# Kernel optimization log

Hardware: AMD Instinct MI355X
Metric: run time of the kernel (lower is better)

Reference implementation:

```python
import jax, jax.numpy as jnp
import numpy as np

B, C_IN, C_OUT, N, K = 4, 128, 128, 4096, 32
BN_EPS = 1e-5


def setup_inputs() -> dict:
    key = jax.random.key(0)
    ks = jax.random.split(key, 12)
    x = jax.random.normal(ks[0], (B, C_IN, N), jnp.float32)
    feature = jax.random.normal(ks[1], (B, C_OUT, N, K), jnp.float32)
    graph_index = jax.random.randint(ks[2], (B, N, K), 0, N)
    s_in = 1.0 / np.sqrt(C_IN)
    s_out = 1.0 / np.sqrt(C_OUT)
    # theta_x: Conv2d(C_IN -> C_IN, 1x1), shared for theta and phi branches
    Wt = jax.random.uniform(ks[3], (C_IN, C_IN), jnp.float32, -s_in, s_in)
    bt = jax.random.uniform(ks[4], (C_IN,), jnp.float32, -s_in, s_in)
    # g: Conv2d(C_OUT -> C_OUT, 1x1)
    Wg = jax.random.uniform(ks[5], (C_OUT, C_OUT), jnp.float32, -s_out, s_out)
    bg = jax.random.uniform(ks[6], (C_OUT,), jnp.float32, -s_out, s_out)
    # W: Conv1d(C_OUT -> C_OUT, 1) followed by BatchNorm1d(C_OUT)
    Ww = jax.random.uniform(ks[7], (C_OUT, C_OUT), jnp.float32, -s_out, s_out)
    bw = jax.random.uniform(ks[8], (C_OUT,), jnp.float32, -s_out, s_out)
    gamma = jnp.ones((C_OUT,), jnp.float32)
    beta = jnp.zeros((C_OUT,), jnp.float32)
    return {"graph_index": graph_index, "x": x, "feature": feature,
            "Wt": Wt, "bt": bt, "Wg": Wg, "bg": bg,
            "Ww": Ww, "bw": bw, "gamma": gamma, "beta": beta}


def reference(graph_index, x, feature, Wt, bt, Wg, bg, Ww, bw, gamma, beta):
    b, c, n = x.shape
    # torch does x.contiguous().view(B, N, C) -> a reshape, not a transpose
    xr = x.reshape(b, n, c)                                   # [B,N,C]
    # index_points: per-batch gather of k neighbors
    batch_idx = jnp.arange(b)[:, None, None]
    nb = xr[batch_idx, graph_index]                           # [B,N,K,C]
    # theta_x 1x1 conv applied to centre and to neighbors (shared weights)
    theta = jnp.einsum('bnc,dc->bnd', xr, Wt) + bt            # [B,N,C]
    phi = jnp.einsum('bnkc,dc->bnkd', nb, Wt) + bt            # [B,N,K,C]
    # local attention logits over k neighbors, softmax over k
    logits = jnp.einsum('bnd,bnkd->bnk', theta, phi)          # [B,N,K]
    coef = jax.nn.softmax(logits, axis=-1)                    # [B,N,K]
    # g 1x1 conv on neighbor value features
    gx = jnp.einsum('bcnk,dc->bnkd', feature, Wg) + bg        # [B,N,K,Cout]
    # weighted aggregation over neighbors
    out = jnp.einsum('bnk,bnkd->bnd', coef, gx)               # [B,N,Cout]
    # W: 1x1 Conv1d then BatchNorm1d (training-mode batch stats)
    y = jnp.einsum('bnd,ed->ben', out, Ww) + bw[None, :, None]  # [B,Cout,N]
    mean = jnp.mean(y, axis=(0, 2), keepdims=True)
    var = jnp.var(y, axis=(0, 2), keepdims=True)
    z = (y - mean) * jax.lax.rsqrt(var + BN_EPS)
    z = z * gamma[None, :, None] + beta[None, :, None]
    return z
```

## Files before the change

kernel.cpp:

```cpp
#include <hip/hip_runtime.h>
#include <hip/hip_bf16.h>

#define BB 4
#define CC 128
#define NN 4096
#define KK 32
#define THETA_OFF 0
#define THETA_SZ  (BB*NN*CC)
#define AGG_OFF   (THETA_OFF + THETA_SZ)
#define AGG_SZ    (BB*NN*CC)
#define M_OFF     (AGG_OFF + AGG_SZ)
#define M_SZ      (CC*CC)
#define B2_OFF    (M_OFF + M_SZ)
#define COEF_OFF  (B2_OFF + 128)
#define COEF_SZ   (BB*NN*KK)
#define PART_OFF  (COEF_OFF + COEF_SZ)
#define PART_SZ   (512*256)
#define PART2_OFF (PART_OFF + PART_SZ)
#define PART2_SZ  (64*256)

__device__ __forceinline__ float dot4(float4 a, float4 b) {
    return a.x*b.x + a.y*b.y + a.z*b.z + a.w*b.w;
}

__device__ __forceinline__ void async_copy16(const float* g, float* l) {
    __builtin_amdgcn_global_load_lds(
        (const __attribute__((address_space(1))) void*)g,
        (__attribute__((address_space(3))) void*)l, 16, 0, 0);
}

__global__ __launch_bounds__(256) void kWT(const float* __restrict__ x,
                                           const float* __restrict__ Wt,
                                           const float* __restrict__ bt,
                                           const float* __restrict__ Ww,
                                           const float* __restrict__ Wg,
                                           const float* __restrict__ bg,
                                           const float* __restrict__ bw,
                                           float* __restrict__ theta,
                                           float* __restrict__ M,
                                           float* __restrict__ b2) {
    __shared__ float xr[32][132];
    __shared__ float wt[128][36];
    int t = threadIdx.x;
    if (blockIdx.x >= 512) {
        int bid2 = blockIdx.x - 512;
        if (bid2 < 64) {
            int e = bid2 * 2 + (t >> 7);
            int c = t & 127;
            float acc = 0.f;
#pragma unroll 8
            for (int d = 0; d < 128; ++d)
                acc += Ww[e*128 + d] * Wg[d*128 + c];
            M[e*128 + c] = acc;
        } else if (t < 128) {
            float acc = bw[t];
            for (int d = 0; d < 128; ++d)
                acc += Ww[t*128 + d] * bg[d];
            b2[t] = acc;
        }
        return;
    }
    long base = (long)blockIdx.x * (32 * 128);
#pragma unroll
    for (int r = 0; r < 4; ++r) {
        int f = (t + 256*r) * 4;
        int dn = f >> 7, c = f & 127;
        *(float4*)&xr[dn][c] = *(const float4*)(x + base + f);
    }
    float acc[4][4] = {};
    int e0 = t & 31, dn0 = (t >> 5) * 4;
    for (int cb = 0; cb < 4; ++cb) {
        __syncthreads();
#pragma unroll
        for (int r = 0; r < 4; ++r) {
            int f = (t + 256*r) * 4;
            int d = f >> 5, cc = f & 31;
            *(float4*)&wt[d][cc] = *(const float4*)(Wt + d*128 + cb*32 + cc);
        }
        __syncthreads();
#pragma unroll
        for (int q = 0; q < 8; ++q) {
            float4 a4[4], m4[4];
#pragma unroll
            for (int j = 0; j < 4; ++j) a4[j] = *(const float4*)&xr[dn0+j][cb*32 + q*4];
#pragma unroll
            for (int i = 0; i < 4; ++i) m4[i] = *(const float4*)&wt[e0 + 32*i][q*4];
#pragma unroll
            for (int i = 0; i < 4; ++i)
#pragma unroll
                for (int j = 0; j < 4; ++j)
                    acc[i][j] += dot4(a4[j], m4[i]);
        }
    }
    __syncthreads();
#pragma unroll
    for (int i = 0; i < 4; ++i) {
        float b = bt[e0 + 32*i];
#pragma unroll
        for (int j = 0; j < 4; ++j)
            xr[dn0 + j][e0 + 32*i] = acc[i][j] + b;
    }
    __syncthreads();
#pragma unroll
    for (int r = 0; r < 4; ++r) {
        int f = (t + 256*r) * 4;
        int dn = f >> 7, c = f & 127;
        *(float4*)(theta + base + f) = *(const float4*)&xr[dn][c];
    }
}

__global__ __launch_bounds__(256) void kA(const int* __restrict__ gi,
                                          const float* __restrict__ theta,
                                          float* __restrict__ coefG) {
    __shared__ float tc[8][132];
    __shared__ float logits[8][33];
    int t = threadIdx.x;
    int bid = (blockIdx.x & 7) * 256 + (blockIdx.x >> 3);
    long trow0 = (long)bid * 8;
    int b = bid >> 9;
    int k = t >> 3, l8 = t & 7;
    {
        int f = t * 4;
        int dn = f >> 7, c = f & 127;
        *(float4*)&tc[dn][c] = *(const float4*)(theta + trow0*128 + f);
    }
    int idxs[8];
#pragma unroll
    for (int dn = 0; dn < 8; ++dn)
        idxs[dn] = gi[(trow0 + dn) * KK + k];
    __syncthreads();
    const float* tbat = theta + (long)b * NN * CC;
#pragma unroll 2
    for (int dn = 0; dn < 8; ++dn) {
        const float* row = tbat + (long)idxs[dn] * CC;
        float p = 0.f;
#pragma unroll
        for (int j = 0; j < 4; ++j) {
            int c = j*32 + l8*4;
            float4 g = *(const float4*)(row + c);
            float4 tcv = *(const float4*)&tc[dn][c];
            p += dot4(g, tcv);
        }
        p += __shfl_xor(p, 1);
        p += __shfl_xor(p, 2);
        p += __shfl_xor(p, 4);
        if (l8 == 0) logits[dn][k] = p;
    }
    __syncthreads();
    if (t < 64) {
        int row = t >> 3;
        float l[4];
#pragma unroll
        for (int j = 0; j < 4; ++j) l[j] = logits[row][l8 + 8*j];
        float m = fmaxf(fmaxf(l[0], l[1]), fmaxf(l[2], l[3]));
        m = fmaxf(m, __shfl_xor(m, 1));
        m = fmaxf(m, __shfl_xor(m, 2));
        m = fmaxf(m, __shfl_xor(m, 4));
        float e[4]; float s = 0.f;
#pragma unroll
        for (int j = 0; j < 4; ++j) { e[j] = __expf(l[j] - m); s += e[j]; }
        s += __shfl_xor(s, 1);
        s += __shfl_xor(s, 2);
        s += __shfl_xor(s, 4);
        float inv = 1.0f / s;
#pragma unroll
        for (int j = 0; j < 4; ++j)
            coefG[(trow0 + row) * KK + l8 + 8*j] = e[j] * inv;
    }
}

__global__ __launch_bounds__(256) void kB(const float* __restrict__ coefG,
                                          const float* __restrict__ feat,
                                          float* __restrict__ aggG) {
    __shared__ float stage[4][2][32][32];
    __shared__ float aggL[32][36];
    int t = threadIdx.x;
    int cc4 = blockIdx.x & 3;
    int tile = blockIdx.x >> 2;
    int b = tile >> 7;
    int n0 = (tile & 127) * 32;
    int w = t >> 6, lane = t & 63;
    int row = lane >> 1, kh = lane & 1;

    const float* cfp = coefG + ((size_t)tile * 32 + row) * KK + kh * 16;
    float4 cf0 = *(const float4*)(cfp);
    float4 cf1 = *(const float4*)(cfp + 4);
    float4 cf2 = *(const float4*)(cfp + 8);
    float4 cf3 = *(const float4*)(cfp + 12);
    asm volatile("" :: "v"(cf0.x), "v"(cf0.y), "v"(cf0.z), "v"(cf0.w));
    asm volatile("" :: "v"(cf1.x), "v"(cf1.y), "v"(cf1.z), "v"(cf1.w));
    asm volatile("" :: "v"(cf2.x), "v"(cf2.y), "v"(cf2.z), "v"(cf2.w));
    asm volatile("" :: "v"(cf3.x), "v"(cf3.y), "v"(cf3.z), "v"(cf3.w));

    const size_t S = (size_t)NN * KK;
    const float* fbase = feat + ((size_t)b * CC + cc4 * 32) * S + (size_t)n0 * KK + lane * 4;
    float* myStage = &stage[w][0][0][0];

#pragma unroll
    for (int ch = 0; ch < 2; ++ch) {
        const float* fc = fbase + (size_t)(ch * 4 + w) * S;
        float* ld = myStage + ch * 1024;
#pragma unroll
        for (int i = 0; i < 4; ++i)
            async_copy16(fc + i * 256, ld + i * 256);
    }

#pragma unroll
    for (int ch = 0; ch < 8; ++ch) {
        if (ch < 7) asm volatile("s_waitcnt vmcnt(4)" ::: "memory");
        else        asm volatile("s_waitcnt vmcnt(0)" ::: "memory");
        const float* sl = myStage + (ch & 1) * 1024 + row * 32 + kh * 16;
        float4 f0 = *(const float4*)(sl);
        float4 f1 = *(const float4*)(sl + 4);
        float4 f2 = *(const float4*)(sl + 8);
        float4 f3 = *(const float4*)(sl + 12);
        float v = dot4(f0, cf0) + dot4(f1, cf1) + dot4(f2, cf2) + dot4(f3, cf3);
        v += __shfl_xor(v, 1);
        if (kh == 0) aggL[row][ch * 4 + w] = v;
        if (ch + 2 < 8) {
            const float* fc = fbase + (size_t)((ch + 2) * 4 + w) * S;
            float* ld = myStage + (ch & 1) * 1024;
#pragma unroll
            for (int i = 0; i < 4; ++i)
                async_copy16(fc + i * 256, ld + i * 256);
        }
    }
    __syncthreads();
    int orow = t >> 3, col4 = (t & 7) * 4;
    *(float4*)(aggG + ((size_t)b * NN + n0 + orow) * CC + cc4 * 32 + col4) =
        *(const float4*)&aggL[orow][col4];
}

__global__ __launch_bounds__(256) void kC(const float* __restrict__ aggG,
                                          const float* __restrict__ Mmat,
                                          const float* __restrict__ b2v,
                                          float* __restrict__ y,
                                          float* __restrict__ partial) {
    __shared__ float agg[32][132];
    __shared__ float mc[128][36];
    __shared__ float pw[4][128];
    __shared__ float qw[4][128];
    int t = threadIdx.x;
    int b = blockIdx.x >> 7;
    int n0 = (blockIdx.x & 127) * 32;
    long base = (long)blockIdx.x * (32 * 128);
#pragma unroll
    for (int r = 0; r < 4; ++r) {
        int f = (t + 256*r) * 4;
        int dn = f >> 7, c = f & 127;
        *(float4*)&agg[dn][c] = *(const float4*)(aggG + base + f);
    }
    float acc[4][4] = {};
    int e0 = t & 31, dn0 = (t >> 5) * 4;
    for (int cb = 0; cb < 4; ++cb) {
        __syncthreads();
#pragma unroll
        for (int r = 0; r < 4; ++r) {
            int f = (t + 256*r) * 4;
            int e = f >> 5, cc = f & 31;
            *(float4*)&mc[e][cc] = *(const float4*)(Mmat + e*128 + cb*32 + cc);
        }
        __syncthreads();
#pragma unroll
        for (int q = 0; q < 8; ++q) {
            float4 a4[4], m4[4];
#pragma unroll
            for (int j = 0; j < 4; ++j) a4[j] = *(const float4*)&agg[dn0+j][cb*32 + q*4];
#pragma unroll
            for (int i = 0; i < 4; ++i) m4[i] = *(const float4*)&mc[e0 + 32*i][q*4];
#pragma unroll
            for (int i = 0; i < 4; ++i)
#pragma unroll
                for (int j = 0; j < 4; ++j)
                    acc[i][j] += dot4(a4[j], m4[i]);
        }
        __syncthreads();
    }
    int w = t >> 6;
#pragma unroll
    for (int i = 0; i < 4; ++i) {
        int e = e0 + 32*i;
        float bb = b2v[e];
        float4 yv;
        yv.x = acc[i][0] + bb;
        yv.y = acc[i][1] + bb;
        yv.z = acc[i][2] + bb;
        yv.w = acc[i][3] + bb;
        *(float4*)(y + ((long)(b*CC + e)) * NN + n0 + dn0) = yv;
        float s = yv.x + yv.y + yv.z + yv.w;
        float qq = yv.x*yv.x + yv.y*yv.y + yv.z*yv.z + yv.w*yv.w;
        s  += __shfl_xor(s, 32);
        qq += __shfl_xor(qq, 32);
        if (!(t & 32)) { pw[w][e] = s; qw[w][e] = qq; }
    }
    __syncthreads();
    if (t < 128) {
        partial[(long)blockIdx.x * 256 + t]       = pw[0][t] + pw[1][t] + pw[2][t] + pw[3][t];
        partial[(long)blockIdx.x * 256 + 128 + t] = qw[0][t] + qw[1][t] + qw[2][t] + qw[3][t];
    }
}

__global__ __launch_bounds__(256) void kR1(const float* __restrict__ partial,
                                           float* __restrict__ partial2) {
    int t = threadIdx.x;
    long b0 = (long)blockIdx.x * 8;
    float acc = 0.f;
#pragma unroll
    for (int j = 0; j < 8; ++j)
        acc += partial[(b0 + j) * 256 + t];
    partial2[(long)blockIdx.x * 256 + t] = acc;
}

__global__ __launch_bounds__(256) void kZf(float* __restrict__ y,
                                           const float* __restrict__ partial2,
                                           const float* __restrict__ gamma,
                                           const float* __restrict__ beta) {
    __shared__ float buf[256];
    __shared__ float scs[128];
    __shared__ float shs[128];
    int t = threadIdx.x;
    float acc = 0.f;
#pragma unroll 8
    for (int j = 0; j < 64; ++j)
        acc += partial2[j * 256 + t];
    buf[t] = acc;
    __syncthreads();
    if (t < 128) {
        float S = buf[t], Q = buf[t + 128];
        const float invN = 1.0f / (BB * NN);
        float mean = S * invN;
        float var  = Q * invN - mean * mean;
        float sc = rsqrtf(var + 1e-5f) * gamma[t];
        scs[t] = sc;
        shs[t] = beta[t] - mean * sc;
    }
    __syncthreads();
    int idx = blockIdx.x * 256 + t;
#pragma unroll
    for (int r = 0; r < 2; ++r) {
        int i = idx + r * 262144;
        int e = (i >> 10) & 127;
        float sc = scs[e], sh = shs[e];
        float4 v = ((float4*)y)[i];
        v.x = v.x * sc + sh;
        v.y = v.y * sc + sh;
        v.z = v.z * sc + sh;
        v.w = v.w * sc + sh;
        ((float4*)y)[i] = v;
    }
}

extern "C" void kernel_launch(void* const* d_in, const int* in_sizes, int n_in,
                              void* d_out, int out_size, void* d_ws, size_t ws_size,
                              hipStream_t stream) {
    const int*   gi    = (const int*)d_in[0];
    const float* x     = (const float*)d_in[1];
    const float* feat  = (const float*)d_in[2];
    const float* Wt    = (const float*)d_in[3];
    const float* bt    = (const float*)d_in[4];
    const float* Wg    = (const float*)d_in[5];
    const float* bg    = (const float*)d_in[6];
    const float* Ww    = (const float*)d_in[7];
    const float* bw    = (const float*)d_in[8];
    const float* gamma = (const float*)d_in[9];
    const float* beta  = (const float*)d_in[10];

    float* y  = (float*)d_out;
    float* ws = (float*)d_ws;
    float* theta    = ws + THETA_OFF;
    float* aggG     = ws + AGG_OFF;
    float* Mmat     = ws + M_OFF;
    float* b2       = ws + B2_OFF;
    float* coefG    = ws + COEF_OFF;
    float* partial  = ws + PART_OFF;
    float* partial2 = ws + PART2_OFF;

    kWT<<<577, 256, 0, stream>>>(x, Wt, bt, Ww, Wg, bg, bw, theta, Mmat, b2);
    kA<<<2048, 256, 0, stream>>>(gi, theta, coefG);
    kB<<<2048, 256, 0, stream>>>(coefG, feat, aggG);
    kC<<<512, 256, 0, stream>>>(aggG, Mmat, b2, y, partial);
    kR1<<<64, 256, 0, stream>>>(partial, partial2);
    kZf<<<1024, 256, 0, stream>>>(y, partial2, gamma, beta);
}
```

Baseline: 101.3 us.

## Fuse neighbor aggregation with output projection and per-tile BN partial sums

Merges the coefficient-weighted feature aggregation kernel and the Ww projection kernel into one kernel. Each block now handles 8 points across all 128 channels and streams features through a 4-deep async LDS ring. This drops the global round trip of the aggregated tensor and one launch. In exchange, every block reloads the full M matrix for only 8 rows of work, the BN partial buffer and its first reduction grow fourfold, and the y stores become narrower per row.

Result: slower. 147.5 us (+45.6%).

```diff
diff --git a/kernel.cpp b/kernel.cpp
--- a/kernel.cpp
+++ b/kernel.cpp
@@ -7,15 +7,13 @@
 #define KK 32
 #define THETA_OFF 0
 #define THETA_SZ  (BB*NN*CC)
-#define AGG_OFF   (THETA_OFF + THETA_SZ)
-#define AGG_SZ    (BB*NN*CC)
-#define M_OFF     (AGG_OFF + AGG_SZ)
+#define M_OFF     (THETA_OFF + THETA_SZ)
 #define M_SZ      (CC*CC)
 #define B2_OFF    (M_OFF + M_SZ)
 #define COEF_OFF  (B2_OFF + 128)
 #define COEF_SZ   (BB*NN*KK)
 #define PART_OFF  (COEF_OFF + COEF_SZ)
-#define PART_SZ   (512*256)
+#define PART_SZ   (2048*256)
 #define PART2_OFF (PART_OFF + PART_SZ)
 #define PART2_SZ  (64*256)
 
@@ -169,144 +167,108 @@
     }
 }
 
-__global__ __launch_bounds__(256) void kB(const float* __restrict__ coefG,
-                                          const float* __restrict__ feat,
-                                          float* __restrict__ aggG) {
-    __shared__ float stage[4][2][32][32];
-    __shared__ float aggL[32][36];
-    int t = threadIdx.x;
-    int cc4 = blockIdx.x & 3;
-    int tile = blockIdx.x >> 2;
-    int b = tile >> 7;
-    int n0 = (tile & 127) * 32;
+union SH8 {
+    float ring[4][4][256];
+    float mc[128][36];
+    float yT[128][8];
+};
+
+__global__ __launch_bounds__(256) void kBC8(const float* __restrict__ coefG,
+                                            const float* __restrict__ feat,
+                                            const float* __restrict__ Mmat,
+                                            const float* __restrict__ b2v,
+                                            float* __restrict__ y,
+                                            float* __restrict__ partial) {
+    __shared__ SH8 sh;
+    __shared__ float aggL[8][132];
+    int t = threadIdx.x;
+    int tile8 = (blockIdx.x & 7) * 256 + (blockIdx.x >> 3);
+    int b = tile8 >> 9;
+    int n0 = (tile8 & 511) * 8;
     int w = t >> 6, lane = t & 63;
-    int row = lane >> 1, kh = lane & 1;
-
-    const float* cfp = coefG + ((size_t)tile * 32 + row) * KK + kh * 16;
-    float4 cf0 = *(const float4*)(cfp);
-    float4 cf1 = *(const float4*)(cfp + 4);
-    float4 cf2 = *(const float4*)(cfp + 8);
-    float4 cf3 = *(const float4*)(cfp + 12);
-    asm volatile("" :: "v"(cf0.x), "v"(cf0.y), "v"(cf0.z), "v"(cf0.w));
-    asm volatile("" :: "v"(cf1.x), "v"(cf1.y), "v"(cf1.z), "v"(cf1.w));
-    asm volatile("" :: "v"(cf2.x), "v"(cf2.y), "v"(cf2.z), "v"(cf2.w));
-    asm volatile("" :: "v"(cf3.x), "v"(cf3.y), "v"(cf3.z), "v"(cf3.w));
+    int row = lane >> 3, koct = lane & 7;
+
+    float4 cf = *(const float4*)(coefG + (size_t)tile8 * 256 + lane * 4);
+    asm volatile("" :: "v"(cf.x), "v"(cf.y), "v"(cf.z), "v"(cf.w));
 
     const size_t S = (size_t)NN * KK;
-    const float* fbase = feat + ((size_t)b * CC + cc4 * 32) * S + (size_t)n0 * KK + lane * 4;
-    float* myStage = &stage[w][0][0][0];
-
-#pragma unroll
-    for (int ch = 0; ch < 2; ++ch) {
-        const float* fc = fbase + (size_t)(ch * 4 + w) * S;
-        float* ld = myStage + ch * 1024;
-#pragma unroll
-        for (int i = 0; i < 4; ++i)
-            async_copy16(fc + i * 256, ld + i * 256);
-    }
-
-#pragma unroll
-    for (int ch = 0; ch < 8; ++ch) {
-        if (ch < 7) asm volatile("s_waitcnt vmcnt(4)" ::: "memory");
-        else        asm volatile("s_waitcnt vmcnt(0)" ::: "memory");
-        const float* sl = myStage + (ch & 1) * 1024 + row * 32 + kh * 16;
-        float4 f0 = *(const float4*)(sl);
-        float4 f1 = *(const float4*)(sl + 4);
-        float4 f2 = *(const float4*)(sl + 8);
-        float4 f3 = *(const float4*)(sl + 12);
-        float v = dot4(f0, cf0) + dot4(f1, cf1) + dot4(f2, cf2) + dot4(f3, cf3);
+    const float* fbase = feat + ((size_t)b * CC + w) * S + (size_t)n0 * KK + lane * 4;
+
+#pragma unroll
+    for (int ch = 0; ch < 4; ++ch)
+        async_copy16(fbase + (size_t)(ch * 4) * S, &sh.ring[ch][w][0]);
+
+#pragma unroll
+    for (int ch = 0; ch < 32; ++ch) {
+        if (ch < 29)       asm volatile("s_waitcnt vmcnt(3)" ::: "memory");
+        else if (ch == 29) asm volatile("s_waitcnt vmcnt(2)" ::: "memory");
+        else if (ch == 30) asm volatile("s_waitcnt vmcnt(1)" ::: "memory");
+        else               asm volatile("s_waitcnt vmcnt(0)" ::: "memory");
+        float4 f = *(const float4*)&sh.ring[ch & 3][w][lane * 4];
+        float v = dot4(f, cf);
         v += __shfl_xor(v, 1);
-        if (kh == 0) aggL[row][ch * 4 + w] = v;
-        if (ch + 2 < 8) {
-            const float* fc = fbase + (size_t)((ch + 2) * 4 + w) * S;
-            float* ld = myStage + (ch & 1) * 1024;
-#pragma unroll
-            for (int i = 0; i < 4; ++i)
-                async_copy16(fc + i * 256, ld + i * 256);
-        }
-    }
-    __syncthreads();
-    int orow = t >> 3, col4 = (t & 7) * 4;
-    *(float4*)(aggG + ((size_t)b * NN + n0 + orow) * CC + cc4 * 32 + col4) =
-        *(const float4*)&aggL[orow][col4];
-}
-
-__global__ __launch_bounds__(256) void kC(const float* __restrict__ aggG,
-                                          const float* __restrict__ Mmat,
-                                          const float* __restrict__ b2v,
-                                          float* __restrict__ y,
-                                          float* __restrict__ partial) {
-    __shared__ float agg[32][132];
-    __shared__ float mc[128][36];
-    __shared__ float pw[4][128];
-    __shared__ float qw[4][128];
-    int t = threadIdx.x;
-    int b = blockIdx.x >> 7;
-    int n0 = (blockIdx.x & 127) * 32;
-    long base = (long)blockIdx.x * (32 * 128);
-#pragma unroll
-    for (int r = 0; r < 4; ++r) {
-        int f = (t + 256*r) * 4;
-        int dn = f >> 7, c = f & 127;
-        *(float4*)&agg[dn][c] = *(const float4*)(aggG + base + f);
-    }
-    float acc[4][4] = {};
-    int e0 = t & 31, dn0 = (t >> 5) * 4;
+        v += __shfl_xor(v, 2);
+        v += __shfl_xor(v, 4);
+        if (koct == 0) aggL[row][ch * 4 + w] = v;
+        if (ch + 4 < 32) {
+            asm volatile("s_waitcnt lgkmcnt(0)" ::: "memory");
+            async_copy16(fbase + (size_t)((ch + 4) * 4) * S, &sh.ring[ch & 3][w][0]);
+        }
+    }
+    __syncthreads();
+
+    float acc[4] = {0.f, 0.f, 0.f, 0.f};
+    int e0 = t & 31, dn0 = t >> 5;
     for (int cb = 0; cb < 4; ++cb) {
         __syncthreads();
 #pragma unroll
         for (int r = 0; r < 4; ++r) {
             int f = (t + 256*r) * 4;
             int e = f >> 5, cc = f & 31;
-            *(float4*)&mc[e][cc] = *(const float4*)(Mmat + e*128 + cb*32 + cc);
+            *(float4*)&sh.mc[e][cc] = *(const float4*)(Mmat + e*128 + cb*32 + cc);
         }
         __syncthreads();
 #pragma unroll
         for (int q = 0; q < 8; ++q) {
-            float4 a4[4], m4[4];
-#pragma unroll
-            for (int j = 0; j < 4; ++j) a4[j] = *(const float4*)&agg[dn0+j][cb*32 + q*4];
-#pragma unroll
-            for (int i = 0; i < 4; ++i) m4[i] = *(const float4*)&mc[e0 + 32*i][q*4];
-#pragma unroll
-            for (int i = 0; i < 4; ++i)
-#pragma unroll
-                for (int j = 0; j < 4; ++j)
-                    acc[i][j] += dot4(a4[j], m4[i]);
-        }
-        __syncthreads();
-    }
-    int w = t >> 6;
+            float4 a4 = *(const float4*)&aggL[dn0][cb*32 + q*4];
+#pragma unroll
+            for (int i = 0; i < 4; ++i) {
+                float4 m4 = *(const float4*)&sh.mc[e0 + 32*i][q*4];
+                acc[i] += dot4(a4, m4);
+            }
+        }
+    }
+    __syncthreads();
 #pragma unroll
     for (int i = 0; i < 4; ++i) {
         int e = e0 + 32*i;
-        float bb = b2v[e];
-        float4 yv;
-        yv.x = acc[i][0] + bb;
-        yv.y = acc[i][1] + bb;
-        yv.z = acc[i][2] + bb;
-        yv.w = acc[i][3] + bb;
-        *(float4*)(y + ((long)(b*CC + e)) * NN + n0 + dn0) = yv;
-        float s = yv.x + yv.y + yv.z + yv.w;
-        float qq = yv.x*yv.x + yv.y*yv.y + yv.z*yv.z + yv.w*yv.w;
-        s  += __shfl_xor(s, 32);
-        qq += __shfl_xor(qq, 32);
-        if (!(t & 32)) { pw[w][e] = s; qw[w][e] = qq; }
-    }
-    __syncthreads();
+        sh.yT[e][dn0] = acc[i] + b2v[e];
+    }
+    __syncthreads();
+    {
+        int e = t >> 1, half = t & 1;
+        float4 v = *(const float4*)&sh.yT[e][half * 4];
+        *(float4*)(y + ((size_t)(b*CC + e)) * NN + n0 + half*4) = v;
+    }
     if (t < 128) {
-        partial[(long)blockIdx.x * 256 + t]       = pw[0][t] + pw[1][t] + pw[2][t] + pw[3][t];
-        partial[(long)blockIdx.x * 256 + 128 + t] = qw[0][t] + qw[1][t] + qw[2][t] + qw[3][t];
+        float s = 0.f, q = 0.f;
+#pragma unroll
+        for (int j = 0; j < 8; ++j) {
+            float v = sh.yT[t][j];
+            s += v; q += v * v;
+        }
+        partial[(size_t)blockIdx.x * 256 + t]       = s;
+        partial[(size_t)blockIdx.x * 256 + 128 + t] = q;
     }
 }
 
 __global__ __launch_bounds__(256) void kR1(const float* __restrict__ partial,
                                            float* __restrict__ partial2) {
     int t = threadIdx.x;
-    long b0 = (long)blockIdx.x * 8;
+    long b0 = (long)blockIdx.x * 32;
     float acc = 0.f;
-#pragma unroll
-    for (int j = 0; j < 8; ++j)
+#pragma unroll 8
+    for (int j = 0; j < 32; ++j)
         acc += partial[(b0 + j) * 256 + t];
     partial2[(long)blockIdx.x * 256 + t] = acc;
 }
@@ -368,7 +330,6 @@
     float* y  = (float*)d_out;
     float* ws = (float*)d_ws;
     float* theta    = ws + THETA_OFF;
-    float* aggG     = ws + AGG_OFF;
     float* Mmat     = ws + M_OFF;
     float* b2       = ws + B2_OFF;
     float* coefG    = ws + COEF_OFF;
@@ -377,8 +338,7 @@
 
     kWT<<<577, 256, 0, stream>>>(x, Wt, bt, Ww, Wg, bg, bw, theta, Mmat, b2);
     kA<<<2048, 256, 0, stream>>>(gi, theta, coefG);
-    kB<<<2048, 256, 0, stream>>>(coefG, feat, aggG);
-    kC<<<512, 256, 0, stream>>>(aggG, Mmat, b2, y, partial);
+    kBC8<<<2048, 256, 0, stream>>>(coefG, feat, Mmat, b2, y, partial);
     kR1<<<64, 256, 0, stream>>>(partial, partial2);
     kZf<<<1024, 256, 0, stream>>>(y, partial2, gamma, beta);
 }
```
